# Optimization experiments

Measured on AMD Instinct MI355X. Metric: run time of the kernel, lower is better.

The kernel has to match this reference:

```python
import jax, jax.numpy as jnp
import numpy as np

HEADS = 16
D_MODEL = 1024
HEAD_DIM = D_MODEL // HEADS


def setup_inputs() -> dict:
    key = jax.random.key(0)
    ks = jax.random.split(key, 11)
    B, S, D = 2, 2048, D_MODEL
    s = 1.0 / np.sqrt(D)
    inp = {
        'Q': jax.random.normal(ks[0], (B, S, D), jnp.float32),
        'K': jax.random.normal(ks[1], (B, S, D), jnp.float32),
        'V': jax.random.normal(ks[2], (B, S, D), jnp.float32),
        'Wq': jax.random.normal(ks[3], (D, D), jnp.float32) * s,
        'Wk': jax.random.normal(ks[4], (D, D), jnp.float32) * s,
        'Wv': jax.random.normal(ks[5], (D, D), jnp.float32) * s,
        'Wo': jax.random.normal(ks[6], (D, D), jnp.float32) * s,
        'bq': jnp.zeros((D,), jnp.float32),
        'bk': jnp.zeros((D,), jnp.float32),
        'bv': jnp.zeros((D,), jnp.float32),
        'bo': jnp.zeros((D,), jnp.float32),
    }
    return inp


def reference(Q, K, V, Wq, Wk, Wv, Wo, bq, bk, bv, bo):
    B, S, D = Q.shape
    H, Dh = HEADS, HEAD_DIM
    # projections (torch Linear: x @ W.T + b)
    q = (Q @ Wq.T + bq).reshape(B, S, H, Dh).transpose(0, 2, 1, 3)  # [B,H,S,Dh]
    k = (K @ Wk.T + bk).reshape(B, S, H, Dh).transpose(0, 2, 1, 3)
    v = (V @ Wv.T + bv).reshape(B, S, H, Dh).transpose(0, 2, 1, 3)
    # naive scaled dot-product attention, scale = 1/sqrt(head_dim)
    scores = jnp.einsum('bhqd,bhkd->bhqk', q, k) / jnp.sqrt(jnp.float32(Dh))
    attn = jax.nn.softmax(scores, axis=-1)
    out = jnp.einsum('bhqk,bhkd->bhqd', attn, v)
    concat = out.transpose(0, 2, 1, 3).reshape(B, S, D)
    return concat @ Wo.T + bo
```

## Files before the change

### kernel.cpp

```cpp
#include <hip/hip_runtime.h>
#include <hip/hip_bf16.h>


#define SEQ     2048
#define DMODEL  1024
#define NHEADS  16
#define DH      64
#define MROWS   4096
#define M1      (1024*1024)
#define M4      (4*1024*1024)
#define SCQ     0.18033688f

typedef __hip_bfloat16 bf16;
typedef __attribute__((ext_vector_type(8))) short  short8;
typedef __attribute__((ext_vector_type(4))) float  f32x4;

__device__ __forceinline__ bf16 f2b(float x) { return __float2bfloat16(x); }
__device__ __forceinline__ f32x4 mfma16(short8 a, short8 b, f32x4 c) {
    return __builtin_amdgcn_mfma_f32_16x16x32_bf16(a, b, c, 0, 0, 0);
}
__device__ __forceinline__ unsigned pk2(float a, float b) {
    union { __hip_bfloat162 h; unsigned u; } x;
    x.h = __float22bfloat162_rn(float2{a, b});
    return x.u;
}
__device__ __forceinline__ short8 pk8(float4 a, float4 b) {
    union { short8 s; unsigned u[4]; } x;
    x.u[0] = pk2(a.x, a.y); x.u[1] = pk2(a.z, a.w);
    x.u[2] = pk2(b.x, b.y); x.u[3] = pk2(b.z, b.w);
    return x.s;
}
__device__ __forceinline__ float fexp2(float x) {
    return __builtin_amdgcn_exp2f(x);
}

__global__ __launch_bounds__(256) void cvt_all(
    const float* __restrict__ Wq, const float* __restrict__ Wk,
    const float* __restrict__ Wv, const float* __restrict__ Wo,
    const float* __restrict__ Q,  const float* __restrict__ K,
    const float* __restrict__ V,  bf16* __restrict__ dst)
{
    const size_t gid = (size_t)blockIdx.x * 256 + threadIdx.x;
    const size_t e0 = gid * 8;
    const float* s;
    if (e0 < (size_t)4 * M1) {
        const float* w[4] = {Wq, Wk, Wv, Wo};
        s = w[e0 >> 20] + (e0 & (M1 - 1));
    } else {
        const float* a[4] = {nullptr, Q, K, V};
        s = a[e0 >> 22] + (e0 & (M4 - 1));
    }
    float4 x = *(const float4*)s, y = *(const float4*)(s + 4);
    *(short8*)((short*)dst + e0) = pk8(x, y);
}

__global__ __launch_bounds__(256) void cvt_w(
    const float* __restrict__ W0, const float* __restrict__ W1,
    const float* __restrict__ W2, const float* __restrict__ W3,
    bf16* __restrict__ dst)
{
    const int gid = blockIdx.x * 256 + threadIdx.x;
    const int t   = gid >> 17;
    const int off = (gid & 131071) * 8;
    const float* srcs[4] = {W0, W1, W2, W3};
    const float* s = srcs[t] + off;
    float4 a = *(const float4*)s, b = *(const float4*)(s + 4);
    *(short8*)((short*)dst + (size_t)gid * 8) = pk8(a, b);
}

__global__ __launch_bounds__(256) void cvt_1(
    const float* __restrict__ X, bf16* __restrict__ D)
{
    const int gid = blockIdx.x * 256 + threadIdx.x;
    const int off = gid * 8;
    float4 a = *(const float4*)(X + off), b = *(const float4*)(X + off + 4);
    *(short8*)((short*)D + off) = pk8(a, b);
}

template <int BN>
__device__ __forceinline__ void gemm_body(
    const bf16* __restrict__ A, const bf16* __restrict__ B,
    const float* __restrict__ bias, void* __restrict__ outp,
    int m0, int n0, int mode, int bias_m, float scale)
{
    __shared__ short As[128 * 32];
    __shared__ short Bs[BN * 32];
    constexpr int NI = BN / 32;

    const int tid  = threadIdx.x;
    const int lane = tid & 63;
    const int wv   = tid >> 6;
    const int wm   = (wv >> 1) * 64;
    const int wn   = (wv & 1) * (BN / 2);
    const int fn   = lane & 15;
    const int fq   = lane >> 4;

    const int srow = lane >> 2;
    const int scol = (lane & 3) * 8;

    const short* Ag = (const short*)A;
    const short* Bg = (const short*)B;

    f32x4 acc[4][NI];
#pragma unroll
    for (int i = 0; i < 4; ++i)
#pragma unroll
        for (int j = 0; j < NI; ++j) acc[i][j] = (f32x4){0.f, 0.f, 0.f, 0.f};

    for (int k0 = 0; k0 < DMODEL; k0 += 32) {
#pragma unroll
        for (int i = 0; i < 2; ++i) {
            const int rr = wv * 32 + i * 16;
            const short* ga = Ag + (size_t)(m0 + rr + srow) * DMODEL + k0 + scol;
            __builtin_amdgcn_global_load_lds(
                (const __attribute__((address_space(1))) void*)ga,
                (__attribute__((address_space(3))) void*)(As + rr * 32), 16, 0, 0);
        }
#pragma unroll
        for (int i = 0; i < BN / 64; ++i) {
            const int rr = wv * (BN / 4) + i * 16;
            const short* gb = Bg + (size_t)(n0 + rr + srow) * DMODEL + k0 + scol;
            __builtin_amdgcn_global_load_lds(
                (const __attribute__((address_space(1))) void*)gb,
                (__attribute__((address_space(3))) void*)(Bs + rr * 32), 16, 0, 0);
        }
        __syncthreads();

        short8 af[4], bfr[NI];
#pragma unroll
        for (int im = 0; im < 4; ++im)
            af[im] = *(const short8*)(As + (wm + im * 16 + fn) * 32 + fq * 8);
#pragma unroll
        for (int in = 0; in < NI; ++in)
            bfr[in] = *(const short8*)(Bs + (wn + in * 16 + fn) * 32 + fq * 8);
#pragma unroll
        for (int im = 0; im < 4; ++im)
#pragma unroll
            for (int in = 0; in < NI; ++in)
                acc[im][in] = mfma16(af[im], bfr[in], acc[im][in]);
        __syncthreads();
    }

#pragma unroll
    for (int im = 0; im < 4; ++im) {
#pragma unroll
        for (int in = 0; in < NI; ++in) {
#pragma unroll
            for (int r = 0; r < 4; ++r) {
                const int m = m0 + wm + im * 16 + fq * 4 + r;
                const int n = n0 + wn + in * 16 + fn;
                const float c = (acc[im][in][r] + (bias_m ? bias[m] : bias[n])) * scale;
                if (mode == 0) {
                    ((float*)outp)[(size_t)m * DMODEL + n] = c;
                } else if (mode == 1) {
                    const int b = m >> 11, s = m & (SEQ - 1);
                    const int h = n >> 6,  d = n & (DH - 1);
                    ((bf16*)outp)[(((size_t)(b * NHEADS + h) * SEQ) + s) * DH + d] = f2b(c);
                } else {
                    const int h = m >> 6,  d = m & (DH - 1);
                    const int b = n >> 11, s = n & (SEQ - 1);
                    const int p = s & 31;
                    const int sp = (s & ~31) | ((p & 12) << 1) | ((p & 16) >> 2) | (p & 3);
                    ((bf16*)outp)[(((size_t)(b * NHEADS + h) * DH) + d) * SEQ + sp] = f2b(c);
                }
            }
        }
    }
}

__global__ __launch_bounds__(256, 3) void gemm_one(
    const bf16* A, const bf16* B, const float* bias, void* out,
    int mode, int bias_m, float scale)
{
    gemm_body<128>(A, B, bias, out, blockIdx.x * 128, blockIdx.y * 128,
                   mode, bias_m, scale);
}

__global__ __launch_bounds__(256, 3) void gemm_fin(
    const bf16* A, const bf16* B, const float* bias, void* out)
{
    gemm_body<64>(A, B, bias, out, blockIdx.x * 128, blockIdx.y * 64, 0, 0, 1.f);
}

__global__ __launch_bounds__(256, 3) void gemm_qkv(
    const bf16* Qb, const bf16* Kb, const bf16* Vb, const bf16* Wb,
    const float* bq, const float* bk, const float* bv,
    bf16* qp, bf16* kp, bf16* vp)
{
    const int blk = blockIdx.x;
    const int z = blk >> 8, t = blk & 255;
    if (z == 0)
        gemm_body<128>(Qb, Wb,          bq, qp, (t >> 3) * 128, (t & 7) * 128, 1, 0, SCQ);
    else if (z == 1)
        gemm_body<128>(Kb, Wb + M1,     bk, kp, (t >> 3) * 128, (t & 7) * 128, 1, 0, 1.f);
    else
        gemm_body<128>(Wb + 2 * M1, Vb, bv, vp, (t >> 5) * 128, (t & 31) * 128, 2, 1, 1.f);
}

__global__ __launch_bounds__(256) void attn_mfma(
    const bf16* __restrict__ q,
    const bf16* __restrict__ k,
    const bf16* __restrict__ vt,
    bf16* __restrict__ out)
{
    __shared__ short Kt[2][64 * 64];
    __shared__ short Vt[2][64 * 64];

    const int tid  = threadIdx.x;
    const int wave = tid >> 6;
    const int lane = tid & 63;
    const int n    = lane & 15;
    const int quad = lane >> 4;

    const int blk  = blockIdx.x;
    const int xcd  = blk & 7;
    const int rest = blk >> 3;
    const int qt   = rest & 15;
    const int bh   = ((rest >> 4) << 3) | xcd;
    const int q0w  = qt * 128 + wave * 32;

    const bf16* qhead = q  + (size_t)bh * SEQ * DH;
    const bf16* khead = k  + (size_t)bh * SEQ * DH;
    const bf16* vhead = vt + (size_t)bh * DH * SEQ;

    short8 qf[2][2];
#pragma unroll
    for (int qg = 0; qg < 2; ++qg) {
        const short* qr = (const short*)(qhead + (size_t)(q0w + qg * 16 + n) * DH);
        qf[qg][0] = *(const short8*)(qr + quad * 8);
        qf[qg][1] = *(const short8*)(qr + 32 + quad * 8);
    }

    const short8 onesv = {(short)0x3F80, (short)0x3F80, (short)0x3F80, (short)0x3F80,
                          (short)0x3F80, (short)0x3F80, (short)0x3F80, (short)0x3F80};
    const f32x4 Zv = (f32x4){0.f, 0.f, 0.f, 0.f};

    f32x4 O[4][2];
#pragma unroll
    for (int gd = 0; gd < 4; ++gd)
#pragma unroll
        for (int qg = 0; qg < 2; ++qg) O[gd][qg] = Zv;
    f32x4 lacc[2] = {Zv, Zv};

    const int srow = lane >> 3;
    const int schk = (lane & 7) ^ srow;

    auto stage = [&](int kt, int buf) {
        const int kbase = kt * 64;
#pragma unroll
        for (int i = 0; i < 2; ++i) {
            const int r = wave * 16 + i * 8 + srow;
            const char* gk = (const char*)(khead + (size_t)(kbase + r) * DH) + schk * 16;
            const char* gv = (const char*)(vhead + (size_t)r * SEQ + kbase) + schk * 16;
            __builtin_amdgcn_global_load_lds(
                (const __attribute__((address_space(1))) void*)gk,
                (__attribute__((address_space(3))) void*)(Kt[buf] + (wave * 16 + i * 8) * 64),
                16, 0, 0);
            __builtin_amdgcn_global_load_lds(
                (const __attribute__((address_space(1))) void*)gv,
                (__attribute__((address_space(3))) void*)(Vt[buf] + (wave * 16 + i * 8) * 64),
                16, 0, 0);
        }
    };

    stage(0, 0);

    for (int kt = 0; kt < SEQ / 64; ++kt) {
        const int cur = kt & 1;
        __syncthreads();
        if (kt + 1 < SEQ / 64) stage(kt + 1, cur ^ 1);

        const short* KtB = Kt[cur];
        const short* VtB = Vt[cur];

        f32x4 st[4][2];
#pragma unroll
        for (int g = 0; g < 4; ++g) {
            const short* kr = KtB + (g * 16 + n) * 64;
            short8 kf0 = *(const short8*)(kr + ((quad       ^ (n & 7)) * 8));
            short8 kf1 = *(const short8*)(kr + (((4 + quad) ^ (n & 7)) * 8));
#pragma unroll
            for (int qg = 0; qg < 2; ++qg) {
                f32x4 s = mfma16(kf0, qf[qg][0], Zv);
                s = mfma16(kf1, qf[qg][1], s);
                st[g][qg] = s;
            }
        }

        short8 bP[2][2];
#pragma unroll
        for (int t = 0; t < 2; ++t) {
#pragma unroll
            for (int qg = 0; qg < 2; ++qg) {
                union { short8 s8; unsigned u[4]; } bb;
                bb.u[0] = pk2(fexp2(st[2*t][qg][0]),   fexp2(st[2*t][qg][1]));
                bb.u[1] = pk2(fexp2(st[2*t][qg][2]),   fexp2(st[2*t][qg][3]));
                bb.u[2] = pk2(fexp2(st[2*t+1][qg][0]), fexp2(st[2*t+1][qg][1]));
                bb.u[3] = pk2(fexp2(st[2*t+1][qg][2]), fexp2(st[2*t+1][qg][3]));
                bP[t][qg] = bb.s8;
                lacc[qg] = mfma16(onesv, bP[t][qg], lacc[qg]);
            }
        }

#pragma unroll
        for (int gd = 0; gd < 4; ++gd) {
            const short* vr = VtB + (gd * 16 + n) * 64;
#pragma unroll
            for (int t = 0; t < 2; ++t) {
                short8 vf = *(const short8*)(vr + (((t * 4 + quad) ^ (n & 7)) * 8));
#pragma unroll
                for (int qg = 0; qg < 2; ++qg)
                    O[gd][qg] = mfma16(vf, bP[t][qg], O[gd][qg]);
            }
        }
    }

    const float inv0 = 1.0f / lacc[0][0];
    const float inv1 = 1.0f / lacc[1][0];
    const int b = bh >> 4;
    const int h = bh & (NHEADS - 1);
#pragma unroll
    for (int gd = 0; gd < 4; ++gd) {
#pragma unroll
        for (int qg = 0; qg < 2; ++qg) {
            const float iv = qg ? inv1 : inv0;
            const int s = q0w + qg * 16 + n;
            uint2 o;
            o.x = pk2(O[gd][qg][0] * iv, O[gd][qg][1] * iv);
            o.y = pk2(O[gd][qg][2] * iv, O[gd][qg][3] * iv);
            *(uint2*)(out + ((size_t)(b * SEQ + s)) * DMODEL + h * DH + gd * 16 + quad * 4) = o;
        }
    }
}

extern "C" void kernel_launch(void* const* d_in, const int* in_sizes, int n_in,
                              void* d_out, int out_size, void* d_ws, size_t ws_size,
                              hipStream_t stream) {
    const float* Q  = (const float*)d_in[0];
    const float* K  = (const float*)d_in[1];
    const float* V  = (const float*)d_in[2];
    const float* Wq = (const float*)d_in[3];
    const float* Wk = (const float*)d_in[4];
    const float* Wv = (const float*)d_in[5];
    const float* Wo = (const float*)d_in[6];
    const float* bq = (const float*)d_in[7];
    const float* bk = (const float*)d_in[8];
    const float* bv = (const float*)d_in[9];
    const float* bo = (const float*)d_in[10];

    bf16* kp = (bf16*)d_out;
    bf16* vp = kp + M4;

    dim3 bb(256);
    dim3 gqk(MROWS / 128, DMODEL / 128);
    dim3 gvv(DMODEL / 128, MROWS / 128);
    dim3 gfin(MROWS / 128, DMODEL / 64);

    if (ws_size >= (size_t)40 * 1024 * 1024) {
        bf16* Wb = (bf16*)d_ws;
        bf16* Qb = Wb + 4 * M1;
        bf16* Kb = Qb + M4;
        bf16* Vb = Kb + M4;
        bf16* qp = Vb + M4;
        bf16* ao = Qb;

        cvt_all<<<8192, bb, 0, stream>>>(Wq, Wk, Wv, Wo, Q, K, V, Wb);
        gemm_qkv<<<768, bb, 0, stream>>>(Qb, Kb, Vb, Wb, bq, bk, bv, qp, kp, vp);
        attn_mfma<<<512, bb, 0, stream>>>(qp, kp, vp, ao);
        gemm_fin<<<gfin, bb, 0, stream>>>(ao, Wb + 3 * M1, bo, d_out);
    } else {
        bf16* Wb = (bf16*)d_ws;
        bf16* Xb = Wb + 4 * M1;
        bf16* qp = Xb + M4;
        bf16* ao = Xb;

        cvt_w<<<2048, bb, 0, stream>>>(Wq, Wk, Wv, Wo, Wb);
        cvt_1<<<2048, bb, 0, stream>>>(Q, Xb);
        gemm_one<<<gqk, bb, 0, stream>>>(Xb, Wb, bq, qp, 1, 0, SCQ);
        cvt_1<<<2048, bb, 0, stream>>>(K, Xb);
        gemm_one<<<gqk, bb, 0, stream>>>(Xb, Wb + M1, bk, kp, 1, 0, 1.f);
        cvt_1<<<2048, bb, 0, stream>>>(V, Xb);
        gemm_one<<<gvv, bb, 0, stream>>>(Wb + 2 * M1, Xb, bv, vp, 2, 1, 1.f);
        attn_mfma<<<512, bb, 0, stream>>>(qp, kp, vp, ao);
        gemm_fin<<<gfin, bb, 0, stream>>>(ao, Wb + 3 * M1, bo, d_out);
    }
}
```

Before: 223.1 us.

## Double-buffer GEMM LDS tiles and unroll attention loop by two

The GEMM body now keeps two LDS buffers, so the global-to-LDS load of the next K slice overlaps the MFMA work on the current one, and it drops one barrier per step. The attention loop is manually unrolled by two with fixed buffer indices and precomputed swizzle offsets. The final GEMM is launched on a 1D grid with the n-tile varying fastest, which changes block order and L2 reuse of A rows. Doubling the GEMM shared memory may lower occupancy under launch_bounds(256,3).

```diff
diff --git a/kernel.cpp b/kernel.cpp
--- a/kernel.cpp
+++ b/kernel.cpp
@@ -33,6 +33,9 @@
 __device__ __forceinline__ float fexp2(float x) {
     return __builtin_amdgcn_exp2f(x);
 }
+#define GLDS(g, l) __builtin_amdgcn_global_load_lds( \
+    (const __attribute__((address_space(1))) void*)(g), \
+    (__attribute__((address_space(3))) void*)(l), 16, 0, 0)
 
 __global__ __launch_bounds__(256) void cvt_all(
     const float* __restrict__ Wq, const float* __restrict__ Wk,
@@ -83,8 +86,8 @@
     const float* __restrict__ bias, void* __restrict__ outp,
     int m0, int n0, int mode, int bias_m, float scale)
 {
-    __shared__ short As[128 * 32];
-    __shared__ short Bs[BN * 32];
+    __shared__ short As[2][128 * 32];
+    __shared__ short Bs[2][BN * 32];
     constexpr int NI = BN / 32;
 
     const int tid  = threadIdx.x;
@@ -107,38 +110,45 @@
 #pragma unroll
         for (int j = 0; j < NI; ++j) acc[i][j] = (f32x4){0.f, 0.f, 0.f, 0.f};
 
-    for (int k0 = 0; k0 < DMODEL; k0 += 32) {
+    auto stage = [&](int k0, int buf) {
 #pragma unroll
         for (int i = 0; i < 2; ++i) {
             const int rr = wv * 32 + i * 16;
             const short* ga = Ag + (size_t)(m0 + rr + srow) * DMODEL + k0 + scol;
-            __builtin_amdgcn_global_load_lds(
-                (const __attribute__((address_space(1))) void*)ga,
-                (__attribute__((address_space(3))) void*)(As + rr * 32), 16, 0, 0);
+            GLDS(ga, As[buf] + rr * 32);
         }
 #pragma unroll
         for (int i = 0; i < BN / 64; ++i) {
             const int rr = wv * (BN / 4) + i * 16;
             const short* gb = Bg + (size_t)(n0 + rr + srow) * DMODEL + k0 + scol;
-            __builtin_amdgcn_global_load_lds(
-                (const __attribute__((address_space(1))) void*)gb,
-                (__attribute__((address_space(3))) void*)(Bs + rr * 32), 16, 0, 0);
-        }
-        __syncthreads();
-
+            GLDS(gb, Bs[buf] + rr * 32);
+        }
+    };
+
+    auto compute = [&](const short* AsB, const short* BsB) {
         short8 af[4], bfr[NI];
 #pragma unroll
         for (int im = 0; im < 4; ++im)
-            af[im] = *(const short8*)(As + (wm + im * 16 + fn) * 32 + fq * 8);
+            af[im] = *(const short8*)(AsB + (wm + im * 16 + fn) * 32 + fq * 8);
 #pragma unroll
         for (int in = 0; in < NI; ++in)
-            bfr[in] = *(const short8*)(Bs + (wn + in * 16 + fn) * 32 + fq * 8);
+            bfr[in] = *(const short8*)(BsB + (wn + in * 16 + fn) * 32 + fq * 8);
 #pragma unroll
         for (int im = 0; im < 4; ++im)
 #pragma unroll
             for (int in = 0; in < NI; ++in)
                 acc[im][in] = mfma16(af[im], bfr[in], acc[im][in]);
+    };
+
+    stage(0, 0);
+#pragma unroll 1
+    for (int k0 = 0; k0 < DMODEL; k0 += 64) {
         __syncthreads();
+        if (k0 + 32 < DMODEL) stage(k0 + 32, 1);
+        compute(As[0], Bs[0]);
+        __syncthreads();
+        if (k0 + 64 < DMODEL) stage(k0 + 64, 0);
+        compute(As[1], Bs[1]);
     }
 
 #pragma unroll
@@ -179,7 +189,8 @@
 __global__ __launch_bounds__(256, 3) void gemm_fin(
     const bf16* A, const bf16* B, const float* bias, void* out)
 {
-    gemm_body<64>(A, B, bias, out, blockIdx.x * 128, blockIdx.y * 64, 0, 0, 1.f);
+    const int b = blockIdx.x;
+    gemm_body<64>(A, B, bias, out, (b >> 4) * 128, (b & 15) * 64, 0, 0, 1.f);
 }
 
 __global__ __launch_bounds__(256, 3) void gemm_qkv(
@@ -244,6 +255,8 @@
 
     const int srow = lane >> 3;
     const int schk = (lane & 7) ^ srow;
+    const int off0 = ((quad       ^ (n & 7)) * 8);
+    const int off1 = (((4 + quad) ^ (n & 7)) * 8);
 
     auto stage = [&](int kt, int buf) {
         const int kbase = kt * 64;
@@ -252,33 +265,18 @@
             const int r = wave * 16 + i * 8 + srow;
             const char* gk = (const char*)(khead + (size_t)(kbase + r) * DH) + schk * 16;
             const char* gv = (const char*)(vhead + (size_t)r * SEQ + kbase) + schk * 16;
-            __builtin_amdgcn_global_load_lds(
-                (const __attribute__((address_space(1))) void*)gk,
-                (__attribute__((address_space(3))) void*)(Kt[buf] + (wave * 16 + i * 8) * 64),
-                16, 0, 0);
-            __builtin_amdgcn_global_load_lds(
-                (const __attribute__((address_space(1))) void*)gv,
-                (__attribute__((address_space(3))) void*)(Vt[buf] + (wave * 16 + i * 8) * 64),
-                16, 0, 0);
+            GLDS(gk, Kt[buf] + (wave * 16 + i * 8) * 64);
+            GLDS(gv, Vt[buf] + (wave * 16 + i * 8) * 64);
         }
     };
 
-    stage(0, 0);
-
-    for (int kt = 0; kt < SEQ / 64; ++kt) {
-        const int cur = kt & 1;
-        __syncthreads();
-        if (kt + 1 < SEQ / 64) stage(kt + 1, cur ^ 1);
-
-        const short* KtB = Kt[cur];
-        const short* VtB = Vt[cur];
-
+    auto tile_body = [&](const short* KtB, const short* VtB) {
         f32x4 st[4][2];
 #pragma unroll
         for (int g = 0; g < 4; ++g) {
             const short* kr = KtB + (g * 16 + n) * 64;
-            short8 kf0 = *(const short8*)(kr + ((quad       ^ (n & 7)) * 8));
-            short8 kf1 = *(const short8*)(kr + (((4 + quad) ^ (n & 7)) * 8));
+            short8 kf0 = *(const short8*)(kr + off0);
+            short8 kf1 = *(const short8*)(kr + off1);
 #pragma unroll
             for (int qg = 0; qg < 2; ++qg) {
                 f32x4 s = mfma16(kf0, qf[qg][0], Zv);
@@ -286,7 +284,6 @@
                 st[g][qg] = s;
             }
         }
-
         short8 bP[2][2];
 #pragma unroll
         for (int t = 0; t < 2; ++t) {
@@ -301,18 +298,28 @@
                 lacc[qg] = mfma16(onesv, bP[t][qg], lacc[qg]);
             }
         }
-
 #pragma unroll
         for (int gd = 0; gd < 4; ++gd) {
             const short* vr = VtB + (gd * 16 + n) * 64;
-#pragma unroll
-            for (int t = 0; t < 2; ++t) {
-                short8 vf = *(const short8*)(vr + (((t * 4 + quad) ^ (n & 7)) * 8));
-#pragma unroll
-                for (int qg = 0; qg < 2; ++qg)
-                    O[gd][qg] = mfma16(vf, bP[t][qg], O[gd][qg]);
+            short8 vf0 = *(const short8*)(vr + off0);
+            short8 vf1 = *(const short8*)(vr + off1);
+#pragma unroll
+            for (int qg = 0; qg < 2; ++qg) {
+                O[gd][qg] = mfma16(vf0, bP[0][qg], O[gd][qg]);
+                O[gd][qg] = mfma16(vf1, bP[1][qg], O[gd][qg]);
             }
         }
+    };
+
+    stage(0, 0);
+#pragma unroll 1
+    for (int kt = 0; kt < SEQ / 64; kt += 2) {
+        __syncthreads();
+        stage(kt + 1, 1);
+        tile_body(Kt[0], Vt[0]);
+        __syncthreads();
+        if (kt + 2 < SEQ / 64) stage(kt + 2, 0);
+        tile_body(Kt[1], Vt[1]);
     }
 
     const float inv0 = 1.0f / lacc[0][0];
@@ -354,7 +361,6 @@
     dim3 bb(256);
     dim3 gqk(MROWS / 128, DMODEL / 128);
     dim3 gvv(DMODEL / 128, MROWS / 128);
-    dim3 gfin(MROWS / 128, DMODEL / 64);
 
     if (ws_size >= (size_t)40 * 1024 * 1024) {
         bf16* Wb = (bf16*)d_ws;
@@ -367,7 +373,7 @@
         cvt_all<<<8192, bb, 0, stream>>>(Wq, Wk, Wv, Wo, Q, K, V, Wb);
         gemm_qkv<<<768, bb, 0, stream>>>(Qb, Kb, Vb, Wb, bq, bk, bv, qp, kp, vp);
         attn_mfma<<<512, bb, 0, stream>>>(qp, kp, vp, ao);
-        gemm_fin<<<gfin, bb, 0, stream>>>(ao, Wb + 3 * M1, bo, d_out);
+        gemm_fin<<<512, bb, 0, stream>>>(ao, Wb + 3 * M1, bo, d_out);
     } else {
         bf16* Wb = (bf16*)d_ws;
         bf16* Xb = Wb + 4 * M1;
@@ -382,6 +388,6 @@
         cvt_1<<<2048, bb, 0, stream>>>(V, Xb);
         gemm_one<<<gvv, bb, 0, stream>>>(Wb + 2 * M1, Xb, bv, vp, 2, 1, 1.f);
         attn_mfma<<<512, bb, 0, stream>>>(qp, kp, vp, ao);
-        gemm_fin<<<gfin, bb, 0, stream>>>(ao, Wb + 3 * M1, bo, d_out);
-    }
-}
+        gemm_fin<<<512, bb, 0, stream>>>(ao, Wb + 3 * M1, bo, d_out);
+    }
+}
```

Result: slower. 228.8 us (+2.5%).
